# Optimization experiments

Hardware: AMD Instinct MI355X
Metric: run time of the kernel (lower is better)

The kernel has to match this reference:

```python
import jax, jax.numpy as jnp
import numpy as np

EPS = 1e-5

def _layernorm(h, g, b):
    m = jnp.mean(h, axis=-1, keepdims=True)
    v = jnp.mean((h - m) ** 2, axis=-1, keepdims=True)
    return (h - m) * jax.lax.rsqrt(v + EPS) * g + b

def setup_inputs() -> dict:
    key = jax.random.key(0)
    ks = jax.random.split(key, 12)
    B, C, T = 8, 512, 8192
    TOK, CD = 256, 768
    s = 0.02
    return {
        "x": jax.random.normal(ks[0], (B, C, T), dtype=jnp.float32),
        "context": jax.random.normal(ks[1], (B, TOK, CD), dtype=jnp.float32),
        "context_mask": jax.random.randint(ks[2], (B, TOK), 0, 2).astype(bool),
        "ln_g": jnp.ones((C,), jnp.float32),
        "ln_b": jnp.zeros((C,), jnp.float32),
        "cln_g": jnp.ones((CD,), jnp.float32),
        "cln_b": jnp.zeros((CD,), jnp.float32),
        "Wq": jax.random.normal(ks[3], (C, C), jnp.float32) * s,
        "bq": jnp.zeros((C,), jnp.float32),
        "Wk": jax.random.normal(ks[4], (C, CD), jnp.float32) * s,
        "bk": jnp.zeros((C,), jnp.float32),
        "Wv": jax.random.normal(ks[5], (C, CD), jnp.float32) * s,
        "bv": jnp.zeros((C,), jnp.float32),
    }

def reference(x, context, context_mask, ln_g, ln_b, cln_g, cln_b, Wq, bq, Wk, bk, Wv, bv):
    H = 8
    B, C, T = x.shape
    TOK = context.shape[1]
    D = C // H
    hidden = jnp.swapaxes(x, 1, 2)                     # [B, T, C]
    q = (_layernorm(hidden, ln_g, ln_b) @ Wq.T + bq).reshape(B, T, H, D)
    ctx_n = _layernorm(context, cln_g, cln_b)          # [B, TOK, CD]
    k = (ctx_n @ Wk.T + bk).reshape(B, TOK, H, D)
    v = (ctx_n @ Wv.T + bv).reshape(B, TOK, H, D)
    q = jax.nn.softmax(q, axis=-1)                     # feature map on queries
    m = context_mask[:, :, None, None]
    k = jnp.where(m, k, -jnp.finfo(k.dtype).max)
    v = v * m.astype(v.dtype)
    k = jax.nn.softmax(k, axis=1)                      # softmax over tokens
    attn = jnp.einsum('bnhd,bnhe->bhde', k, v)         # small [B,H,D,D] context matrix
    out = jnp.einsum('bthd,bhde->bthe', q, attn).reshape(B, T, C)
    return x + jnp.swapaxes(out, 1, 2)
```

## Files before the change

kernel.cpp:

```cpp
#include <hip/hip_runtime.h>

#define B_ 8
#define C_ 512
#define T_ 8192
#define TOK_ 256
#define CD_ 768
#define H_ 8
#define D_ 64

typedef __attribute__((ext_vector_type(8))) short bf16x8;
typedef __attribute__((ext_vector_type(4))) float f32x4;

__device__ __forceinline__ unsigned short f2bf(float f){
  union { float f; unsigned u; } v; v.f = f;
  return (unsigned short)((v.u + 0x7FFFu + ((v.u >> 16) & 1u)) >> 16);
}

__global__ void pack_wq(const float* __restrict__ Wq, unsigned short* __restrict__ out){
  int slot = blockIdx.x * 256 + threadIdx.x;
  int ln = slot & 63, nt = (slot >> 6) & 31, kk = slot >> 11;
  int n  = nt * 16 + (ln & 15);
  int k0 = kk * 32 + (ln >> 4) * 8;
  bf16x8 v;
  #pragma unroll
  for (int j = 0; j < 8; j++) v[j] = (short)f2bf(Wq[(size_t)n * C_ + k0 + j]);
  *(bf16x8*)&out[(size_t)slot * 8] = v;
}

__global__ void ctx_ln(const float* __restrict__ ctx, const float* __restrict__ g,
                       const float* __restrict__ bl, float* __restrict__ outn){
  int row = blockIdx.x;
  const float* p = ctx + (size_t)row * CD_;
  int tid = threadIdx.x;
  float s1 = 0.f, s2 = 0.f;
  for (int i = tid; i < CD_; i += 256){ float v = p[i]; s1 += v; s2 += v * v; }
  #pragma unroll
  for (int o = 32; o > 0; o >>= 1){ s1 += __shfl_xor(s1, o); s2 += __shfl_xor(s2, o); }
  __shared__ float rs[4][2];
  if ((tid & 63) == 0){ rs[tid >> 6][0] = s1; rs[tid >> 6][1] = s2; }
  __syncthreads();
  s1 = rs[0][0] + rs[1][0] + rs[2][0] + rs[3][0];
  s2 = rs[0][1] + rs[1][1] + rs[2][1] + rs[3][1];
  float m = s1 / (float)CD_;
  float var = s2 / (float)CD_ - m * m;
  float rstd = rsqrtf(var + 1e-5f);
  float* q = outn + (size_t)row * CD_;
  for (int i = tid; i < CD_; i += 256) q[i] = (p[i] - m) * rstd * g[i] + bl[i];
}

__global__ __launch_bounds__(256) void kv_gemm(const float* __restrict__ ctxn,
    const float* __restrict__ Wk, const float* __restrict__ Wv,
    const float* __restrict__ bk, const float* __restrict__ bv,
    const int* __restrict__ mask, float* __restrict__ kv){
  __shared__ float As[32][68];
  __shared__ float Bs[32][68];
  int tid = threadIdx.x;
  int n0 = blockIdx.x * 64;
  int m0 = blockIdx.y * 64;
  const float* W = (n0 < 512) ? Wk : Wv;
  int nc0 = n0 & 511;
  float acc[4][4] = {};
  int tx = tid & 15, ty = tid >> 4;
  for (int ks = 0; ks < CD_; ks += 32){
    __syncthreads();
    #pragma unroll
    for (int e = 0; e < 8; e++){
      int el = e * 256 + tid;
      int k_l = el & 31, m_l = el >> 5;
      As[k_l][m_l] = ctxn[(size_t)(m0 + m_l) * CD_ + ks + k_l];
      Bs[k_l][m_l] = W[(size_t)(nc0 + m_l) * CD_ + ks + k_l];
    }
    __syncthreads();
    #pragma unroll 4
    for (int k = 0; k < 32; k++){
      float av[4], bv2[4];
      #pragma unroll
      for (int i = 0; i < 4; i++) av[i]  = As[k][ty * 4 + i];
      #pragma unroll
      for (int j = 0; j < 4; j++) bv2[j] = Bs[k][tx * 4 + j];
      #pragma unroll
      for (int i = 0; i < 4; i++)
        #pragma unroll
        for (int j = 0; j < 4; j++)
          acc[i][j] = fmaf(av[i], bv2[j], acc[i][j]);
    }
  }
  #pragma unroll
  for (int i = 0; i < 4; i++){
    int m = m0 + ty * 4 + i;
    int bb = m >> 8, ntok = m & 255;
    bool msk = mask[bb * 256 + ntok] != 0;
    #pragma unroll
    for (int j = 0; j < 4; j++){
      int n = n0 + tx * 4 + j;
      float v = acc[i][j];
      if (n < 512) v = msk ? (v + bk[n]) : -3.402823466e38f;
      else         v = msk ? (v + bv[n - 512]) : 0.0f;
      kv[(size_t)m * 1024 + n] = v;
    }
  }
}

__global__ __launch_bounds__(256) void attn_build(const float* __restrict__ kv,
                                                  unsigned short* __restrict__ apk){
  __shared__ float kl[TOK_ * 64];
  __shared__ float vl[TOK_ * 64];
  __shared__ float al[64 * 64];
  __shared__ float sc[256];
  __shared__ float mx_l[64], inv_l[64];
  int tid = threadIdx.x;
  int b = blockIdx.x >> 3, h = blockIdx.x & 7;
  for (int e = 0; e < 64; e++){
    int el = e * 256 + tid;
    int n = el >> 6, d = el & 63;
    kl[n * 64 + d] = kv[(size_t)(b * 256 + n) * 1024 + h * 64 + d];
    vl[n * 64 + d] = kv[(size_t)(b * 256 + n) * 1024 + 512 + h * 64 + d];
  }
  __syncthreads();
  int d = tid >> 2, q = tid & 3;
  float mx = -3.402823466e38f;
  for (int j = 0; j < 64; j++) mx = fmaxf(mx, kl[(q * 64 + j) * 64 + d]);
  sc[d * 4 + q] = mx;
  __syncthreads();
  if (tid < 64) mx_l[tid] = fmaxf(fmaxf(sc[tid*4], sc[tid*4+1]), fmaxf(sc[tid*4+2], sc[tid*4+3]));
  __syncthreads();
  float mv = mx_l[d];
  float s = 0.f;
  for (int j = 0; j < 64; j++){
    int n = q * 64 + j;
    float p = expf(kl[n * 64 + d] - mv);
    kl[n * 64 + d] = p;
    s += p;
  }
  sc[d * 4 + q] = s;
  __syncthreads();
  if (tid < 64) inv_l[tid] = 1.0f / (sc[tid*4] + sc[tid*4+1] + sc[tid*4+2] + sc[tid*4+3]);
  __syncthreads();
  float a[16] = {};
  for (int n = 0; n < 256; n++){
    float wv = kl[n * 64 + d];
    #pragma unroll
    for (int j = 0; j < 16; j++) a[j] = fmaf(wv, vl[n * 64 + q * 16 + j], a[j]);
  }
  float inv = inv_l[d];
  #pragma unroll
  for (int j = 0; j < 16; j++) al[d * 64 + q * 16 + j] = a[j] * inv;
  __syncthreads();
  #pragma unroll
  for (int s2 = 0; s2 < 2; s2++){
    int slot = s2 * 256 + tid;
    int ln = slot & 63, nt = (slot >> 6) & 3, kk = slot >> 8;
    int e = nt * 16 + (ln & 15), d0 = kk * 32 + (ln >> 4) * 8;
    bf16x8 v;
    #pragma unroll
    for (int j = 0; j < 8; j++) v[j] = (short)f2bf(al[(d0 + j) * 64 + e]);
    *(bf16x8*)&apk[((size_t)(b * 8 + h) * 512 + slot) * 8] = v;
  }
}

__global__ __launch_bounds__(256, 2) void fused_main(const float* __restrict__ x,
    const float* __restrict__ g, const float* __restrict__ bl,
    const unsigned short* __restrict__ wq_pk, const float* __restrict__ bq,
    const unsigned short* __restrict__ attn_pk, float* __restrict__ out){
  __shared__ unsigned short a_lds[32 * 512];
  __shared__ _Float16 x_l[512 * 32];
  __shared__ float red[32 * 8 * 2];
  __shared__ float m_l[32], rs_l[32];
  const int tid = threadIdx.x;
  const int b = blockIdx.y;
  const int t0 = blockIdx.x * 32;
  const float* xb = x + (size_t)b * C_ * T_ + t0;

  {
    int t = tid & 31, cg = tid >> 5;
    float s1 = 0.f, s2 = 0.f;
    for (int j = 0; j < 64; j++){
      int c = cg * 64 + j;
      float v = xb[(size_t)c * T_ + t];
      s1 += v; s2 += v * v;
      x_l[c * 32 + t] = (_Float16)v;
    }
    red[(t * 8 + cg) * 2 + 0] = s1;
    red[(t * 8 + cg) * 2 + 1] = s2;
  }
  __syncthreads();
  if (tid < 32){
    float s1 = 0.f, s2 = 0.f;
    for (int j = 0; j < 8; j++){ s1 += red[(tid*8+j)*2]; s2 += red[(tid*8+j)*2+1]; }
    float m = s1 * (1.0f / 512.0f);
    float var = s2 * (1.0f / 512.0f) - m * m;
    m_l[tid] = m;
    rs_l[tid] = rsqrtf(var + 1e-5f);
  }
  __syncthreads();
  {
    int t = tid & 31, cg = tid >> 5;
    float m = m_l[t], rs = rs_l[t];
    for (int o = 0; o < 8; o++){
      int c0 = cg * 64 + o * 8;
      bf16x8 av;
      #pragma unroll
      for (int j = 0; j < 8; j++){
        int c = c0 + j;
        float v = (float)x_l[c * 32 + t];
        av[j] = (short)f2bf((v - m) * rs * g[c] + bl[c]);
      }
      *(bf16x8*)&a_lds[(t * 512 + c0) ^ ((t & 7) << 3)] = av;
    }
  }
  __syncthreads();

  const int w = tid >> 6, ln = tid & 63, lc = ln & 15, lk = ln >> 4;
  f32x4 acc[2][8];
  #pragma unroll
  for (int i = 0; i < 2; i++)
    #pragma unroll
    for (int j = 0; j < 8; j++) acc[i][j] = (f32x4){0.f, 0.f, 0.f, 0.f};
  const bf16x8* wqv = (const bf16x8*)wq_pk;
  bf16x8 bbuf[2][8];
  #pragma unroll
  for (int nt = 0; nt < 8; nt++) bbuf[0][nt] = wqv[(size_t)(0 * 32 + w * 8 + nt) * 64 + ln];
  #pragma unroll
  for (int kk = 0; kk < 16; kk++){
    int cur = kk & 1, nxt = cur ^ 1;
    if (kk < 15){
      #pragma unroll
      for (int nt = 0; nt < 8; nt++)
        bbuf[nxt][nt] = wqv[(size_t)((kk + 1) * 32 + w * 8 + nt) * 64 + ln];
    }
    bf16x8 af[2];
    #pragma unroll
    for (int mt = 0; mt < 2; mt++){
      int t = mt * 16 + lc;
      af[mt] = *(const bf16x8*)&a_lds[(t * 512 + kk * 32 + lk * 8) ^ ((t & 7) << 3)];
    }
    #pragma unroll
    for (int mt = 0; mt < 2; mt++)
      #pragma unroll
      for (int nt = 0; nt < 8; nt++)
        acc[mt][nt] = __builtin_amdgcn_mfma_f32_16x16x32_bf16(af[mt], bbuf[cur][nt], acc[mt][nt], 0, 0, 0);
  }
  bf16x8 b2[2][2][4];
  const bf16x8* apk = (const bf16x8*)attn_pk;
  #pragma unroll
  for (int hh = 0; hh < 2; hh++)
    #pragma unroll
    for (int k2 = 0; k2 < 2; k2++)
      #pragma unroll
      for (int np = 0; np < 4; np++)
        b2[hh][k2][np] = apk[((size_t)(b * 8 + (2 * w + hh)) * 512 + (k2 * 4 + np) * 64 + ln)];
  float bqv[8];
  #pragma unroll
  for (int nt = 0; nt < 8; nt++) bqv[nt] = bq[w * 128 + nt * 16 + lc];
  #pragma unroll
  for (int mt = 0; mt < 2; mt++)
    #pragma unroll
    for (int r = 0; r < 4; r++)
      #pragma unroll
      for (int h2 = 0; h2 < 2; h2++){
        float v[4];
        #pragma unroll
        for (int j = 0; j < 4; j++) v[j] = acc[mt][h2 * 4 + j][r] + bqv[h2 * 4 + j];
        float mx = fmaxf(fmaxf(v[0], v[1]), fmaxf(v[2], v[3]));
        #pragma unroll
        for (int o = 1; o < 16; o <<= 1) mx = fmaxf(mx, __shfl_xor(mx, o));
        float e[4], s = 0.f;
        #pragma unroll
        for (int j = 0; j < 4; j++){ e[j] = expf(v[j] - mx); s += e[j]; }
        #pragma unroll
        for (int o = 1; o < 16; o <<= 1) s += __shfl_xor(s, o);
        float inv = 1.0f / s;
        #pragma unroll
        for (int j = 0; j < 4; j++) acc[mt][h2 * 4 + j][r] = e[j] * inv;
      }
  __syncthreads();
  #pragma unroll
  for (int mt = 0; mt < 2; mt++)
    #pragma unroll
    for (int r = 0; r < 4; r++){
      int t = mt * 16 + lk * 4 + r;
      #pragma unroll
      for (int nt = 0; nt < 8; nt++){
        int col = w * 128 + nt * 16 + lc;
        a_lds[(t * 512 + col) ^ ((t & 7) << 3)] = f2bf(acc[mt][nt][r]);
      }
    }
  __syncthreads();
  f32x4 acc2[2][2][4];
  #pragma unroll
  for (int i = 0; i < 2; i++)
    #pragma unroll
    for (int j = 0; j < 2; j++)
      #pragma unroll
      for (int k = 0; k < 4; k++) acc2[i][j][k] = (f32x4){0.f, 0.f, 0.f, 0.f};
  #pragma unroll
  for (int k2 = 0; k2 < 2; k2++){
    bf16x8 a2[2][2];
    #pragma unroll
    for (int mt = 0; mt < 2; mt++)
      #pragma unroll
      for (int hh = 0; hh < 2; hh++){
        int t = mt * 16 + lc;
        int col = w * 128 + hh * 64 + k2 * 32 + lk * 8;
        a2[mt][hh] = *(const bf16x8*)&a_lds[(t * 512 + col) ^ ((t & 7) << 3)];
      }
    #pragma unroll
    for (int mt = 0; mt < 2; mt++)
      #pragma unroll
      for (int hh = 0; hh < 2; hh++)
        #pragma unroll
        for (int np = 0; np < 4; np++)
          acc2[mt][hh][np] = __builtin_amdgcn_mfma_f32_16x16x32_bf16(a2[mt][hh], b2[hh][k2][np], acc2[mt][hh][np], 0, 0, 0);
  }
  float* trf = (float*)a_lds;
  const int tt = ln & 31, jj = ln >> 5;
  for (int gq = 0; gq < 8; gq++){
    int hh = gq >> 2, np = gq & 3;
    __syncthreads();
    #pragma unroll
    for (int mt = 0; mt < 2; mt++)
      #pragma unroll
      for (int r = 0; r < 4; r++){
        int t = mt * 16 + lk * 4 + r;
        trf[(t * 256 + w * 64 + lc) ^ ((t & 7) << 2)] = acc2[mt][hh][np][r];
      }
    __syncthreads();
    #pragma unroll
    for (int c8 = 0; c8 < 8; c8++){
      int cl = jj * 8 + c8;
      float o = trf[(tt * 256 + w * 64 + cl) ^ ((tt & 7) << 2)];
      int c = w * 128 + hh * 64 + np * 16 + cl;
      float xv = (float)x_l[c * 32 + tt];
      out[((size_t)b * C_ + c) * T_ + t0 + tt] = xv + o;
    }
  }
}

extern "C" void kernel_launch(void* const* d_in, const int* in_sizes, int n_in,
                              void* d_out, int out_size, void* d_ws, size_t ws_size,
                              hipStream_t stream) {
  (void)in_sizes; (void)n_in; (void)out_size; (void)ws_size;
  const float* x     = (const float*)d_in[0];
  const float* ctx   = (const float*)d_in[1];
  const int*   mask  = (const int*)d_in[2];
  const float* ln_g  = (const float*)d_in[3];
  const float* ln_b  = (const float*)d_in[4];
  const float* cln_g = (const float*)d_in[5];
  const float* cln_b = (const float*)d_in[6];
  const float* Wq    = (const float*)d_in[7];
  const float* bq    = (const float*)d_in[8];
  const float* Wk    = (const float*)d_in[9];
  const float* bk    = (const float*)d_in[10];
  const float* Wv    = (const float*)d_in[11];
  const float* bv    = (const float*)d_in[12];
  float* out = (float*)d_out;
  char* wsb = (char*)d_ws;
  float* ctx_n = (float*)wsb;
  float* kv    = (float*)(wsb + 6291456);
  unsigned short* wq_pk   = (unsigned short*)(wsb + 14680064);
  unsigned short* attn_pk = (unsigned short*)(wsb + 15204352);

  pack_wq<<<128, 256, 0, stream>>>(Wq, wq_pk);
  ctx_ln<<<2048, 256, 0, stream>>>(ctx, cln_g, cln_b, ctx_n);
  kv_gemm<<<dim3(16, 32), 256, 0, stream>>>(ctx_n, Wk, Wv, bk, bv, mask, kv);
  attn_build<<<64, 256, 0, stream>>>(kv, attn_pk);
  fused_main<<<dim3(T_ / 32, B_), 256, 0, stream>>>(x, ln_g, ln_b, wq_pk, bq, attn_pk, out);
}
```

Before: 425.4 us.

## Fuse KV projection and context-matrix build into one MFMA kernel, drop x LDS cache

Replaces the scalar fp32 kv_gemm and attn_build kernels with a single per-(batch,head) kernel. It computes K/V with bf16 MFMA from a bf16 layer-normed context and pre-packed Wk/Wv, then does the masked token softmax in registers and the P^T V product with MFMA. In the main kernel the fp16 x copy in LDS is removed and x is re-read from global memory, which frees LDS so occupancy can rise to 3 blocks. The output transpose-store is also restructured with a different swizzle. The costs are extra global reads of x, and bf16 precision in the K/V path that can change the softmax accuracy.

```diff
diff --git a/kernel.cpp b/kernel.cpp
--- a/kernel.cpp
+++ b/kernel.cpp
@@ -5,8 +5,6 @@
 #define T_ 8192
 #define TOK_ 256
 #define CD_ 768
-#define H_ 8
-#define D_ 64
 
 typedef __attribute__((ext_vector_type(8))) short bf16x8;
 typedef __attribute__((ext_vector_type(4))) float f32x4;
@@ -27,8 +25,23 @@
   *(bf16x8*)&out[(size_t)slot * 8] = v;
 }
 
+__global__ void pack_wkv(const float* __restrict__ Wk, const float* __restrict__ Wv,
+                         unsigned short* __restrict__ out){
+  int slot = blockIdx.x * 256 + threadIdx.x;
+  int ln = slot & 63, nt = (slot >> 6) & 7;
+  int kkh = slot >> 9;
+  int kk = kkh % 24, h = kkh / 24;
+  const float* W = (nt < 4) ? Wk : Wv;
+  int row = h * 64 + (nt & 3) * 16 + (ln & 15);
+  int k0 = kk * 32 + (ln >> 4) * 8;
+  bf16x8 v;
+  #pragma unroll
+  for (int j = 0; j < 8; j++) v[j] = (short)f2bf(W[(size_t)row * CD_ + k0 + j]);
+  *(bf16x8*)&out[(size_t)slot * 8] = v;
+}
+
 __global__ void ctx_ln(const float* __restrict__ ctx, const float* __restrict__ g,
-                       const float* __restrict__ bl, float* __restrict__ outn){
+                       const float* __restrict__ bl, unsigned short* __restrict__ outn){
   int row = blockIdx.x;
   const float* p = ctx + (size_t)row * CD_;
   int tid = threadIdx.x;
@@ -44,126 +57,203 @@
   float m = s1 / (float)CD_;
   float var = s2 / (float)CD_ - m * m;
   float rstd = rsqrtf(var + 1e-5f);
-  float* q = outn + (size_t)row * CD_;
-  for (int i = tid; i < CD_; i += 256) q[i] = (p[i] - m) * rstd * g[i] + bl[i];
-}
-
-__global__ __launch_bounds__(256) void kv_gemm(const float* __restrict__ ctxn,
-    const float* __restrict__ Wk, const float* __restrict__ Wv,
+  unsigned short* q = outn + (size_t)row * CD_;
+  for (int i = tid; i < CD_; i += 256) q[i] = f2bf((p[i] - m) * rstd * g[i] + bl[i]);
+}
+
+__global__ __launch_bounds__(256) void ctx_attn(const unsigned short* __restrict__ ctx_nb,
+    const unsigned short* __restrict__ wkv_pk,
     const float* __restrict__ bk, const float* __restrict__ bv,
-    const int* __restrict__ mask, float* __restrict__ kv){
-  __shared__ float As[32][68];
-  __shared__ float Bs[32][68];
-  int tid = threadIdx.x;
-  int n0 = blockIdx.x * 64;
-  int m0 = blockIdx.y * 64;
-  const float* W = (n0 < 512) ? Wk : Wv;
-  int nc0 = n0 & 511;
-  float acc[4][4] = {};
-  int tx = tid & 15, ty = tid >> 4;
-  for (int ks = 0; ks < CD_; ks += 32){
+    const int* __restrict__ mask, unsigned short* __restrict__ apk){
+  __shared__ __align__(16) char smem[75776];
+  unsigned short* a_st  = (unsigned short*)smem;
+  unsigned short* p_lds = (unsigned short*)smem;
+  unsigned short* v_lds = (unsigned short*)(smem + 32768);
+  unsigned short* al    = (unsigned short*)(smem + 65536);
+  float* wred = (float*)(smem + 73728);
+  int* msk_l  = (int*)(smem + 74752);
+
+  const int tid = threadIdx.x;
+  const int b = blockIdx.x >> 3, h = blockIdx.x & 7;
+  msk_l[tid] = mask[b * 256 + tid];
+
+  const unsigned short* cb = ctx_nb + (size_t)b * 256 * CD_;
+  const int w = tid >> 6, ln = tid & 63, lc = ln & 15, lk = ln >> 4;
+
+  {
+    const bf16x8* src = (const bf16x8*)(cb + (size_t)tid * CD_);
+    #pragma unroll
+    for (int s = 0; s < 4; s++){
+      bf16x8 vv = src[s];
+      *(bf16x8*)&a_st[(tid * 32 + s * 8) ^ ((tid & 7) << 3)] = vv;
+    }
+  }
+  const bf16x8* wv_ = (const bf16x8*)wkv_pk;
+  const size_t wbase = (size_t)h * 24 * 8 * 64;
+  f32x4 acc[4][8];
+  #pragma unroll
+  for (int i = 0; i < 4; i++)
+    #pragma unroll
+    for (int j = 0; j < 8; j++) acc[i][j] = (f32x4){0.f,0.f,0.f,0.f};
+  bf16x8 bbuf[2][8];
+  #pragma unroll
+  for (int nt = 0; nt < 8; nt++) bbuf[0][nt] = wv_[wbase + (size_t)(0 * 8 + nt) * 64 + ln];
+  __syncthreads();
+
+  for (int kk = 0; kk < 24; kk++){
+    int cur = kk & 1;
+    if (kk < 23){
+      const bf16x8* src = (const bf16x8*)(cb + (size_t)tid * CD_ + (kk + 1) * 32);
+      unsigned short* dst = a_st + (cur ^ 1) * 8192;
+      #pragma unroll
+      for (int s = 0; s < 4; s++){
+        bf16x8 vv = src[s];
+        *(bf16x8*)&dst[(tid * 32 + s * 8) ^ ((tid & 7) << 3)] = vv;
+      }
+      #pragma unroll
+      for (int nt = 0; nt < 8; nt++)
+        bbuf[cur ^ 1][nt] = wv_[wbase + (size_t)((kk + 1) * 8 + nt) * 64 + ln];
+    }
+    bf16x8 af[4];
+    #pragma unroll
+    for (int mt = 0; mt < 4; mt++){
+      int row = w * 64 + mt * 16 + lc;
+      af[mt] = *(const bf16x8*)&a_st[cur * 8192 + ((row * 32 + lk * 8) ^ ((row & 7) << 3))];
+    }
+    #pragma unroll
+    for (int mt = 0; mt < 4; mt++)
+      #pragma unroll
+      for (int nt = 0; nt < 8; nt++)
+        acc[mt][nt] = __builtin_amdgcn_mfma_f32_16x16x32_bf16(af[mt], bbuf[cur][nt], acc[mt][nt], 0, 0, 0);
     __syncthreads();
-    #pragma unroll
-    for (int e = 0; e < 8; e++){
-      int el = e * 256 + tid;
-      int k_l = el & 31, m_l = el >> 5;
-      As[k_l][m_l] = ctxn[(size_t)(m0 + m_l) * CD_ + ks + k_l];
-      Bs[k_l][m_l] = W[(size_t)(nc0 + m_l) * CD_ + ks + k_l];
-    }
-    __syncthreads();
-    #pragma unroll 4
-    for (int k = 0; k < 32; k++){
-      float av[4], bv2[4];
-      #pragma unroll
-      for (int i = 0; i < 4; i++) av[i]  = As[k][ty * 4 + i];
-      #pragma unroll
-      for (int j = 0; j < 4; j++) bv2[j] = Bs[k][tx * 4 + j];
-      #pragma unroll
-      for (int i = 0; i < 4; i++)
-        #pragma unroll
-        for (int j = 0; j < 4; j++)
-          acc[i][j] = fmaf(av[i], bv2[j], acc[i][j]);
-    }
-  }
-  #pragma unroll
-  for (int i = 0; i < 4; i++){
-    int m = m0 + ty * 4 + i;
-    int bb = m >> 8, ntok = m & 255;
-    bool msk = mask[bb * 256 + ntok] != 0;
-    #pragma unroll
-    for (int j = 0; j < 4; j++){
-      int n = n0 + tx * 4 + j;
-      float v = acc[i][j];
-      if (n < 512) v = msk ? (v + bk[n]) : -3.402823466e38f;
-      else         v = msk ? (v + bv[n - 512]) : 0.0f;
-      kv[(size_t)m * 1024 + n] = v;
-    }
-  }
-}
-
-__global__ __launch_bounds__(256) void attn_build(const float* __restrict__ kv,
-                                                  unsigned short* __restrict__ apk){
-  __shared__ float kl[TOK_ * 64];
-  __shared__ float vl[TOK_ * 64];
-  __shared__ float al[64 * 64];
-  __shared__ float sc[256];
-  __shared__ float mx_l[64], inv_l[64];
-  int tid = threadIdx.x;
-  int b = blockIdx.x >> 3, h = blockIdx.x & 7;
-  for (int e = 0; e < 64; e++){
-    int el = e * 256 + tid;
-    int n = el >> 6, d = el & 63;
-    kl[n * 64 + d] = kv[(size_t)(b * 256 + n) * 1024 + h * 64 + d];
-    vl[n * 64 + d] = kv[(size_t)(b * 256 + n) * 1024 + 512 + h * 64 + d];
-  }
-  __syncthreads();
-  int d = tid >> 2, q = tid & 3;
-  float mx = -3.402823466e38f;
-  for (int j = 0; j < 64; j++) mx = fmaxf(mx, kl[(q * 64 + j) * 64 + d]);
-  sc[d * 4 + q] = mx;
-  __syncthreads();
-  if (tid < 64) mx_l[tid] = fmaxf(fmaxf(sc[tid*4], sc[tid*4+1]), fmaxf(sc[tid*4+2], sc[tid*4+3]));
-  __syncthreads();
-  float mv = mx_l[d];
-  float s = 0.f;
-  for (int j = 0; j < 64; j++){
-    int n = q * 64 + j;
-    float p = expf(kl[n * 64 + d] - mv);
-    kl[n * 64 + d] = p;
-    s += p;
-  }
-  sc[d * 4 + q] = s;
-  __syncthreads();
-  if (tid < 64) inv_l[tid] = 1.0f / (sc[tid*4] + sc[tid*4+1] + sc[tid*4+2] + sc[tid*4+3]);
-  __syncthreads();
-  float a[16] = {};
-  for (int n = 0; n < 256; n++){
-    float wv = kl[n * 64 + d];
-    #pragma unroll
-    for (int j = 0; j < 16; j++) a[j] = fmaf(wv, vl[n * 64 + q * 16 + j], a[j]);
-  }
-  float inv = inv_l[d];
-  #pragma unroll
-  for (int j = 0; j < 16; j++) al[d * 64 + q * 16 + j] = a[j] * inv;
-  __syncthreads();
+  }
+
+  float bia[8];
+  #pragma unroll
+  for (int nt = 0; nt < 8; nt++)
+    bia[nt] = (nt < 4) ? bk[h * 64 + nt * 16 + lc] : bv[h * 64 + (nt - 4) * 16 + lc];
+  bool mk[4][4];
+  #pragma unroll
+  for (int mt = 0; mt < 4; mt++)
+    #pragma unroll
+    for (int r = 0; r < 4; r++)
+      mk[mt][r] = msk_l[w * 64 + mt * 16 + lk * 4 + r] != 0;
+
+  float cred[4];
+  #pragma unroll
+  for (int nt = 0; nt < 4; nt++){
+    float mx = -3.402823466e38f;
+    #pragma unroll
+    for (int mt = 0; mt < 4; mt++)
+      #pragma unroll
+      for (int r = 0; r < 4; r++)
+        if (mk[mt][r]) mx = fmaxf(mx, acc[mt][nt][r] + bia[nt]);
+    mx = fmaxf(mx, __shfl_xor(mx, 16));
+    mx = fmaxf(mx, __shfl_xor(mx, 32));
+    cred[nt] = mx;
+  }
+  if (lk == 0){
+    #pragma unroll
+    for (int nt = 0; nt < 4; nt++) wred[w * 64 + nt * 16 + lc] = cred[nt];
+  }
+  __syncthreads();
+  float gmx[4];
+  #pragma unroll
+  for (int nt = 0; nt < 4; nt++){
+    int d = nt * 16 + lc;
+    gmx[nt] = fmaxf(fmaxf(wred[d], wred[64 + d]), fmaxf(wred[128 + d], wred[192 + d]));
+  }
+  __syncthreads();
+  #pragma unroll
+  for (int nt = 0; nt < 4; nt++){
+    float s = 0.f;
+    #pragma unroll
+    for (int mt = 0; mt < 4; mt++)
+      #pragma unroll
+      for (int r = 0; r < 4; r++){
+        float p = mk[mt][r] ? expf(acc[mt][nt][r] + bia[nt] - gmx[nt]) : 0.f;
+        acc[mt][nt][r] = p;
+        s += p;
+      }
+    s += __shfl_xor(s, 16);
+    s += __shfl_xor(s, 32);
+    cred[nt] = s;
+  }
+  if (lk == 0){
+    #pragma unroll
+    for (int nt = 0; nt < 4; nt++) wred[w * 64 + nt * 16 + lc] = cred[nt];
+  }
+  __syncthreads();
+  float ginv[4];
+  #pragma unroll
+  for (int nt = 0; nt < 4; nt++){
+    int d = nt * 16 + lc;
+    float s = wred[d] + wred[64 + d] + wred[128 + d] + wred[192 + d];
+    ginv[nt] = 1.0f / fmaxf(s, 1e-30f);
+  }
+  #pragma unroll
+  for (int nt = 0; nt < 4; nt++){
+    int d = nt * 16 + lc;
+    #pragma unroll
+    for (int mt = 0; mt < 4; mt++)
+      #pragma unroll
+      for (int r = 0; r < 4; r++){
+        int n = w * 64 + mt * 16 + lk * 4 + r;
+        p_lds[(d * 256 + n) ^ ((d & 7) << 3)] = f2bf(acc[mt][nt][r] * ginv[nt]);
+      }
+  }
+  #pragma unroll
+  for (int nt = 4; nt < 8; nt++){
+    int e = (nt - 4) * 16 + lc;
+    #pragma unroll
+    for (int mt = 0; mt < 4; mt++)
+      #pragma unroll
+      for (int r = 0; r < 4; r++){
+        int n = w * 64 + mt * 16 + lk * 4 + r;
+        float vv = mk[mt][r] ? (acc[mt][nt][r] + bia[nt]) : 0.f;
+        v_lds[(e * 256 + n) ^ ((e & 7) << 3)] = f2bf(vv);
+      }
+  }
+  __syncthreads();
+
+  f32x4 acc2[4];
+  #pragma unroll
+  for (int i = 0; i < 4; i++) acc2[i] = (f32x4){0.f,0.f,0.f,0.f};
+  #pragma unroll
+  for (int kk = 0; kk < 8; kk++){
+    int d = w * 16 + lc;
+    bf16x8 pa = *(const bf16x8*)&p_lds[(d * 256 + kk * 32 + lk * 8) ^ ((d & 7) << 3)];
+    #pragma unroll
+    for (int nt2 = 0; nt2 < 4; nt2++){
+      int e = nt2 * 16 + lc;
+      bf16x8 vb = *(const bf16x8*)&v_lds[(e * 256 + kk * 32 + lk * 8) ^ ((e & 7) << 3)];
+      acc2[nt2] = __builtin_amdgcn_mfma_f32_16x16x32_bf16(pa, vb, acc2[nt2], 0, 0, 0);
+    }
+  }
+  #pragma unroll
+  for (int nt2 = 0; nt2 < 4; nt2++)
+    #pragma unroll
+    for (int r = 0; r < 4; r++)
+      al[(w * 16 + lk * 4 + r) * 64 + nt2 * 16 + lc] = f2bf(acc2[nt2][r]);
+  __syncthreads();
+
   #pragma unroll
   for (int s2 = 0; s2 < 2; s2++){
     int slot = s2 * 256 + tid;
-    int ln = slot & 63, nt = (slot >> 6) & 3, kk = slot >> 8;
-    int e = nt * 16 + (ln & 15), d0 = kk * 32 + (ln >> 4) * 8;
+    int l2 = slot & 63, nt = (slot >> 6) & 3, kk = slot >> 8;
+    int e = nt * 16 + (l2 & 15), d0 = kk * 32 + (l2 >> 4) * 8;
     bf16x8 v;
     #pragma unroll
-    for (int j = 0; j < 8; j++) v[j] = (short)f2bf(al[(d0 + j) * 64 + e]);
+    for (int j = 0; j < 8; j++) v[j] = (short)al[(d0 + j) * 64 + e];
     *(bf16x8*)&apk[((size_t)(b * 8 + h) * 512 + slot) * 8] = v;
   }
 }
 
-__global__ __launch_bounds__(256, 2) void fused_main(const float* __restrict__ x,
+__global__ __launch_bounds__(256, 3) void fused_main(const float* __restrict__ x,
     const float* __restrict__ g, const float* __restrict__ bl,
     const unsigned short* __restrict__ wq_pk, const float* __restrict__ bq,
     const unsigned short* __restrict__ attn_pk, float* __restrict__ out){
   __shared__ unsigned short a_lds[32 * 512];
-  __shared__ _Float16 x_l[512 * 32];
   __shared__ float red[32 * 8 * 2];
   __shared__ float m_l[32], rs_l[32];
   const int tid = threadIdx.x;
@@ -178,7 +268,6 @@
       int c = cg * 64 + j;
       float v = xb[(size_t)c * T_ + t];
       s1 += v; s2 += v * v;
-      x_l[c * 32 + t] = (_Float16)v;
     }
     red[(t * 8 + cg) * 2 + 0] = s1;
     red[(t * 8 + cg) * 2 + 1] = s2;
@@ -186,6 +275,7 @@
   __syncthreads();
   if (tid < 32){
     float s1 = 0.f, s2 = 0.f;
+    #pragma unroll
     for (int j = 0; j < 8; j++){ s1 += red[(tid*8+j)*2]; s2 += red[(tid*8+j)*2+1]; }
     float m = s1 * (1.0f / 512.0f);
     float var = s2 * (1.0f / 512.0f) - m * m;
@@ -202,7 +292,7 @@
       #pragma unroll
       for (int j = 0; j < 8; j++){
         int c = c0 + j;
-        float v = (float)x_l[c * 32 + t];
+        float v = xb[(size_t)c * T_ + t];
         av[j] = (short)f2bf((v - m) * rs * g[c] + bl[c]);
       }
       *(bf16x8*)&a_lds[(t * 512 + c0) ^ ((t & 7) << 3)] = av;
@@ -219,7 +309,7 @@
   const bf16x8* wqv = (const bf16x8*)wq_pk;
   bf16x8 bbuf[2][8];
   #pragma unroll
-  for (int nt = 0; nt < 8; nt++) bbuf[0][nt] = wqv[(size_t)(0 * 32 + w * 8 + nt) * 64 + ln];
+  for (int nt = 0; nt < 8; nt++) bbuf[0][nt] = wqv[(size_t)(w * 8 + nt) * 64 + ln];
   #pragma unroll
   for (int kk = 0; kk < 16; kk++){
     int cur = kk & 1, nxt = cur ^ 1;
@@ -313,24 +403,28 @@
           acc2[mt][hh][np] = __builtin_amdgcn_mfma_f32_16x16x32_bf16(a2[mt][hh], b2[hh][k2][np], acc2[mt][hh][np], 0, 0, 0);
   }
   float* trf = (float*)a_lds;
-  const int tt = ln & 31, jj = ln >> 5;
-  for (int gq = 0; gq < 8; gq++){
-    int hh = gq >> 2, np = gq & 3;
+  const int tt = ln & 31;
+  const int rowid = (w << 1) | (ln >> 5);
+  #pragma unroll
+  for (int hh = 0; hh < 2; hh++){
     __syncthreads();
     #pragma unroll
-    for (int mt = 0; mt < 2; mt++)
-      #pragma unroll
-      for (int r = 0; r < 4; r++){
-        int t = mt * 16 + lk * 4 + r;
-        trf[(t * 256 + w * 64 + lc) ^ ((t & 7) << 2)] = acc2[mt][hh][np][r];
-      }
+    for (int np = 0; np < 4; np++)
+      #pragma unroll
+      for (int mt = 0; mt < 2; mt++)
+        #pragma unroll
+        for (int r = 0; r < 4; r++){
+          int t = mt * 16 + lk * 4 + r;
+          int cc = w * 64 + np * 16 + lc;
+          trf[(t * 256 + cc) ^ (((t & 7) << 2) | ((t >> 3) & 3))] = acc2[mt][hh][np][r];
+        }
     __syncthreads();
     #pragma unroll
-    for (int c8 = 0; c8 < 8; c8++){
-      int cl = jj * 8 + c8;
-      float o = trf[(tt * 256 + w * 64 + cl) ^ ((tt & 7) << 2)];
-      int c = w * 128 + hh * 64 + np * 16 + cl;
-      float xv = (float)x_l[c * 32 + tt];
+    for (int i = 0; i < 32; i++){
+      int cc = i * 8 + rowid;
+      int c = (cc >> 6) * 128 + hh * 64 + (cc & 63);
+      float o = trf[(tt * 256 + cc) ^ (((tt & 7) << 2) | ((tt >> 3) & 3))];
+      float xv = xb[(size_t)c * T_ + tt];
       out[((size_t)b * C_ + c) * T_ + t0 + tt] = xv + o;
     }
   }
@@ -355,14 +449,14 @@
   const float* bv    = (const float*)d_in[12];
   float* out = (float*)d_out;
   char* wsb = (char*)d_ws;
-  float* ctx_n = (float*)wsb;
-  float* kv    = (float*)(wsb + 6291456);
-  unsigned short* wq_pk   = (unsigned short*)(wsb + 14680064);
-  unsigned short* attn_pk = (unsigned short*)(wsb + 15204352);
+  unsigned short* ctx_nb = (unsigned short*)wsb;
+  unsigned short* wq_pk  = (unsigned short*)(wsb + 3145728);
+  unsigned short* wkv_pk = (unsigned short*)(wsb + 3670016);
+  unsigned short* apk    = (unsigned short*)(wsb + 5242880);
 
   pack_wq<<<128, 256, 0, stream>>>(Wq, wq_pk);
-  ctx_ln<<<2048, 256, 0, stream>>>(ctx, cln_g, cln_b, ctx_n);
-  kv_gemm<<<dim3(16, 32), 256, 0, stream>>>(ctx_n, Wk, Wv, bk, bv, mask, kv);
-  attn_build<<<64, 256, 0, stream>>>(kv, attn_pk);
-  fused_main<<<dim3(T_ / 32, B_), 256, 0, stream>>>(x, ln_g, ln_b, wq_pk, bq, attn_pk, out);
-}
+  pack_wkv<<<384, 256, 0, stream>>>(Wk, Wv, wkv_pk);
+  ctx_ln<<<2048, 256, 0, stream>>>(ctx, cln_g, cln_b, ctx_nb);
+  ctx_attn<<<64, 256, 0, stream>>>(ctx_nb, wkv_pk, bk, bv, mask, apk);
+  fused_main<<<dim3(T_ / 32, B_), 256, 0, stream>>>(x, ln_g, ln_b, wq_pk, bq, apk, out);
+}
```

Result: faster. 369.2 us (-13.2%).
